# Kernel tuning notes

Hardware: AMD Instinct MI355X
Metric: run time of the kernel (lower is better)

Reference implementation:

```python
import jax, jax.numpy as jnp
import numpy as np

B, C_IN, C_OUT, E, H, W = 64, 384, 384, 8, 28, 28


def setup_inputs() -> dict:
    key = jax.random.key(0)
    k1, k2, k3 = jax.random.split(key, 3)
    x = jax.random.normal(k1, (B, C_IN, H, W), dtype=jnp.float32)
    routing_weights = jax.random.uniform(k2, (B, E), dtype=jnp.float32)
    # kaiming_normal_(mode='fan_out') per expert: std = sqrt(2 / fan_out), fan_out = out_channels * 1 * 1
    std = float(np.sqrt(2.0 / C_OUT))
    weight = jax.random.normal(k3, (E, C_OUT, C_IN), dtype=jnp.float32) * std
    return {"x": x, "routing_weights": routing_weights, "weight": weight}


def reference(x, routing_weights, weight):
    # Per-sample aggregated 1x1 conv weights: [b, c_out, c_in]
    agg = jnp.einsum('be,eoi->boi', routing_weights, weight)
    # Per-sample channel mixing (1x1 conv with groups=b == batched GEMM)
    out = jnp.einsum('boi,bihw->bohw', agg, x)
    return out
```

## Files before the change

### kernel.cpp

```cpp
#include <hip/hip_runtime.h>
#include <cstdint>

#define B_   64
#define CI_  384
#define CO_  384
#define HW_  784
#define E_   8
#define G_   (CI_ / 8)

typedef unsigned short ushort_t;
typedef unsigned int   uint_t;

typedef __attribute__((ext_vector_type(8))) short bf16x8;
typedef __attribute__((ext_vector_type(4))) float f32x4;

__device__ __forceinline__ ushort_t f2bf_rne(float f) {
  uint_t u = __builtin_bit_cast(uint_t, f);
  u += 0x7fffu + ((u >> 16) & 1u);
  return (ushort_t)(u >> 16);
}

__device__ __forceinline__ uint_t pack_bf16_trunc(float f0, float f1) {
  return __builtin_amdgcn_perm(__builtin_bit_cast(uint_t, f1),
                               __builtin_bit_cast(uint_t, f0),
                               0x07060302u);
}

#define AGG_BLOCKS 288
#define XQ_BLOCKS  (G_ * B_)

__global__ __launch_bounds__(256) void prep(const float* __restrict__ rw,
                                            const float* __restrict__ w,
                                            const float* __restrict__ x,
                                            ushort_t* __restrict__ agg,
                                            ushort_t* __restrict__ xq) {
  __shared__ float r[B_ * E_];
  const int blk = blockIdx.x;
  const int tid = threadIdx.x;

  if (blk < AGG_BLOCKS) {
    r[tid]       = rw[tid];
    r[tid + 256] = rw[tid + 256];
    const int base = blk * 512 + tid * 2;
    float2 wv[E_];
#pragma unroll
    for (int e = 0; e < E_; ++e)
      wv[e] = *(const float2*)&w[e * (CO_ * CI_) + base];
    __syncthreads();
#pragma unroll 8
    for (int b = 0; b < B_; ++b) {
      float ax = 0.f, ay = 0.f;
#pragma unroll
      for (int e = 0; e < E_; ++e) {
        const float rv = r[b * E_ + e];
        ax += rv * wv[e].x;
        ay += rv * wv[e].y;
      }
      const uint_t v = (uint_t)f2bf_rne(ax) | ((uint_t)f2bf_rne(ay) << 16);
      *(uint_t*)&agg[(size_t)b * (CO_ * CI_) + base] = v;
    }
  } else {
    const int idx = blk - AGG_BLOCKS;
    const int g = idx % G_;
    const int b = idx / G_;
    const float* xp = x + ((size_t)b * CI_ + g * 8) * HW_;
    ushort_t* op = xq + (((size_t)b * G_ + g) * HW_) * 8;
#pragma unroll
    for (int c = 0; c < 4; ++c) {
      const int hw = c * 256 + tid;
      if (hw < HW_) {
        float v[8];
#pragma unroll
        for (int j = 0; j < 8; ++j) v[j] = xp[(size_t)j * HW_ + hw];
        uint4 u;
        u.x = pack_bf16_trunc(v[0], v[1]);
        u.y = pack_bf16_trunc(v[2], v[3]);
        u.z = pack_bf16_trunc(v[4], v[5]);
        u.w = pack_bf16_trunc(v[6], v[7]);
        *(uint4*)&op[hw * 8] = u;
      }
    }
  }
}

#define BM 128
#define BN 128
#define BK 32
#define KIT (CI_ / BK)

__global__ __launch_bounds__(256, 4) void moe_gemm3(const ushort_t* __restrict__ Agg,
                                                    const ushort_t* __restrict__ Xq,
                                                    float* __restrict__ Out) {
  __shared__ __align__(16) ushort_t As[2][BM * BK];
  __shared__ __align__(16) ushort_t Bs[2][BN * BK];

  const int tid  = threadIdx.x;
  const int lane = tid & 63;
  const int wave = tid >> 6;
  const int wm = wave & 1, wn = wave >> 1;

  const int bx = blockIdx.x;
  const int by = blockIdx.y;
  const int bg  = by / 21;
  const int rem = by - bg * 21;
  const int mt  = rem / 7;
  const int nt  = rem - mt * 7;
  const int b   = bg * 8 + bx;

  const int sr0 = tid >> 2,          sq0 = (tid & 3) ^ ((tid >> 3) & 3);
  const int sr1 = (tid + 256) >> 2,  sq1 = (tid & 3) ^ (((tid + 256) >> 3) & 3);

  const ushort_t* Ab = Agg + (size_t)b * CO_ * CI_ + (size_t)(mt * BM) * CI_;
  const ushort_t* Asrc0 = Ab + sr0 * CI_ + sq0 * 8;
  const ushort_t* Asrc1 = Ab + sr1 * CI_ + sq1 * 8;

  int hw0 = nt * BN + sr0; hw0 = hw0 < HW_ ? hw0 : HW_ - 1;
  int hw1 = nt * BN + sr1; hw1 = hw1 < HW_ ? hw1 : HW_ - 1;
  const ushort_t* Xb = Xq + (size_t)b * G_ * HW_ * 8;
  const ushort_t* Bsrc0 = Xb + ((size_t)sq0 * HW_ + hw0) * 8;
  const ushort_t* Bsrc1 = Xb + ((size_t)sq1 * HW_ + hw1) * 8;

  const int l15 = lane & 15;
  const int lq  = lane >> 4;
  const int xqA = lq ^ ((l15 >> 1) & 3);

  f32x4 acc[4][4];
#pragma unroll
  for (int i = 0; i < 4; ++i)
#pragma unroll
    for (int j = 0; j < 4; ++j)
      acc[i][j] = (f32x4)0.f;

#define STAGE(PB, KK)                                                          \
  {                                                                            \
    __builtin_amdgcn_global_load_lds(                                          \
        (const __attribute__((address_space(1))) uint_t*)(Asrc0 + (KK) * BK),  \
        (__attribute__((address_space(3))) uint_t*)&As[PB][tid * 8], 16, 0, 0);\
    __builtin_amdgcn_global_load_lds(                                          \
        (const __attribute__((address_space(1))) uint_t*)(Asrc1 + (KK) * BK),  \
        (__attribute__((address_space(3))) uint_t*)&As[PB][(tid + 256) * 8],   \
        16, 0, 0);                                                             \
    const size_t bo_ = (size_t)(KK) * (4 * HW_ * 8);                           \
    __builtin_amdgcn_global_load_lds(                                          \
        (const __attribute__((address_space(1))) uint_t*)(Bsrc0 + bo_),        \
        (__attribute__((address_space(3))) uint_t*)&Bs[PB][tid * 8], 16, 0, 0);\
    __builtin_amdgcn_global_load_lds(                                          \
        (const __attribute__((address_space(1))) uint_t*)(Bsrc1 + bo_),        \
        (__attribute__((address_space(3))) uint_t*)&Bs[PB][(tid + 256) * 8],   \
        16, 0, 0);                                                             \
  }

  STAGE(0, 0);
  __syncthreads();

#pragma unroll 1
  for (int kk = 0; kk < KIT; ++kk) {
    const int buf = kk & 1;
    if (kk + 1 < KIT) STAGE(1 - buf, kk + 1);

    bf16x8 a[4], bb[4];
#pragma unroll
    for (int mf = 0; mf < 4; ++mf) {
      const int row = wm * 64 + mf * 16 + l15;
      a[mf] = *(const bf16x8*)&As[buf][(row * 4 + xqA) * 8];
    }
#pragma unroll
    for (int nf = 0; nf < 4; ++nf) {
      const int col = wn * 64 + nf * 16 + l15;
      bb[nf] = *(const bf16x8*)&Bs[buf][(col * 4 + xqA) * 8];
    }
#pragma unroll
    for (int mf = 0; mf < 4; ++mf)
#pragma unroll
      for (int nf = 0; nf < 4; ++nf)
        acc[mf][nf] = __builtin_amdgcn_mfma_f32_16x16x32_bf16(a[mf], bb[nf],
                                                              acc[mf][nf], 0, 0, 0);
    __syncthreads();
  }

  float* Ob = Out + (size_t)b * CO_ * HW_;
#pragma unroll
  for (int mf = 0; mf < 4; ++mf) {
#pragma unroll
    for (int nf = 0; nf < 4; ++nf) {
      const int n = nt * BN + wn * 64 + nf * 16 + l15;
      if (n < HW_) {
        const int mbase = mt * BM + wm * 64 + mf * 16 + lq * 4;
#pragma unroll
        for (int r = 0; r < 4; ++r)
          Ob[(size_t)(mbase + r) * HW_ + n] = acc[mf][nf][r];
      }
    }
  }
}

extern "C" void kernel_launch(void* const* d_in, const int* in_sizes, int n_in,
                              void* d_out, int out_size, void* d_ws, size_t ws_size,
                              hipStream_t stream) {
  const float* x  = (const float*)d_in[0];
  const float* rw = (const float*)d_in[1];
  const float* w  = (const float*)d_in[2];
  float* out = (float*)d_out;

  ushort_t* agg = (ushort_t*)d_ws;
  ushort_t* xq  = agg + (size_t)B_ * CO_ * CI_;

  prep<<<AGG_BLOCKS + XQ_BLOCKS, 256, 0, stream>>>(rw, w, x, agg, xq);
  moe_gemm3<<<dim3(8, 21 * (B_ / 8)), 256, 0, stream>>>(agg, xq, out);
}
```

Measured before the change: 173.6 us.

## Triple-buffer GEMM K-loop with explicit vmcnt waits and MFMA priority

Replaces the double-buffered K loop with a three-stage LDS ring that keeps two tile loads in flight. Each iteration waits on vmcnt and uses a single barrier in place of two __syncthreads, and the fully unrolled loop uses sched_barrier fences. s_setprio is raised around the MFMA block so matrix work is favoured while loads are pending. The cost is 1.5x the LDS per block and a lower occupancy hint (3 blocks per CU instead of 4).

```diff
diff --git a/kernel.cpp b/kernel.cpp
--- a/kernel.cpp
+++ b/kernel.cpp
@@ -88,11 +88,11 @@
 #define BK 32
 #define KIT (CI_ / BK)
 
-__global__ __launch_bounds__(256, 4) void moe_gemm3(const ushort_t* __restrict__ Agg,
+__global__ __launch_bounds__(256, 3) void moe_gemm4(const ushort_t* __restrict__ Agg,
                                                     const ushort_t* __restrict__ Xq,
                                                     float* __restrict__ Out) {
-  __shared__ __align__(16) ushort_t As[2][BM * BK];
-  __shared__ __align__(16) ushort_t Bs[2][BN * BK];
+  __shared__ __align__(16) ushort_t As[3][BM * BK];
+  __shared__ __align__(16) ushort_t Bs[3][BN * BK];
 
   const int tid  = threadIdx.x;
   const int lane = tid & 63;
@@ -150,33 +150,53 @@
         16, 0, 0);                                                             \
   }
 
+#define COMPUTE(CB)                                                            \
+  {                                                                            \
+    bf16x8 a[4], bb[4];                                                        \
+    _Pragma("unroll") for (int mf = 0; mf < 4; ++mf) {                         \
+      const int row = wm * 64 + mf * 16 + l15;                                 \
+      a[mf] = *(const bf16x8*)&As[CB][(row * 4 + xqA) * 8];                    \
+    }                                                                          \
+    _Pragma("unroll") for (int nf = 0; nf < 4; ++nf) {                         \
+      const int col = wn * 64 + nf * 16 + l15;                                 \
+      bb[nf] = *(const bf16x8*)&Bs[CB][(col * 4 + xqA) * 8];                   \
+    }                                                                          \
+    __builtin_amdgcn_s_setprio(1);                                             \
+    _Pragma("unroll") for (int mf = 0; mf < 4; ++mf)                           \
+      _Pragma("unroll") for (int nf = 0; nf < 4; ++nf)                         \
+        acc[mf][nf] = __builtin_amdgcn_mfma_f32_16x16x32_bf16(a[mf], bb[nf],   \
+                                                              acc[mf][nf],     \
+                                                              0, 0, 0);        \
+    __builtin_amdgcn_s_setprio(0);                                             \
+  }
+
+#define ITER_S(VM, CB, STG)                                                    \
+  {                                                                            \
+    asm volatile("s_waitcnt vmcnt(" #VM ")" ::: "memory");                     \
+    __builtin_amdgcn_s_barrier();                                              \
+    __builtin_amdgcn_sched_barrier(0);                                         \
+    STAGE((STG) % 3, STG);                                                     \
+    COMPUTE(CB);                                                               \
+    __builtin_amdgcn_sched_barrier(0);                                         \
+  }
+#define ITER_N(VM, CB)                                                         \
+  {                                                                            \
+    asm volatile("s_waitcnt vmcnt(" #VM ")" ::: "memory");                     \
+    __builtin_amdgcn_s_barrier();                                              \
+    __builtin_amdgcn_sched_barrier(0);                                         \
+    COMPUTE(CB);                                                               \
+    __builtin_amdgcn_sched_barrier(0);                                         \
+  }
+
   STAGE(0, 0);
-  __syncthreads();
-
-#pragma unroll 1
-  for (int kk = 0; kk < KIT; ++kk) {
-    const int buf = kk & 1;
-    if (kk + 1 < KIT) STAGE(1 - buf, kk + 1);
-
-    bf16x8 a[4], bb[4];
-#pragma unroll
-    for (int mf = 0; mf < 4; ++mf) {
-      const int row = wm * 64 + mf * 16 + l15;
-      a[mf] = *(const bf16x8*)&As[buf][(row * 4 + xqA) * 8];
-    }
-#pragma unroll
-    for (int nf = 0; nf < 4; ++nf) {
-      const int col = wn * 64 + nf * 16 + l15;
-      bb[nf] = *(const bf16x8*)&Bs[buf][(col * 4 + xqA) * 8];
-    }
-#pragma unroll
-    for (int mf = 0; mf < 4; ++mf)
-#pragma unroll
-      for (int nf = 0; nf < 4; ++nf)
-        acc[mf][nf] = __builtin_amdgcn_mfma_f32_16x16x32_bf16(a[mf], bb[nf],
-                                                              acc[mf][nf], 0, 0, 0);
-    __syncthreads();
-  }
+  STAGE(1, 1);
+
+#pragma unroll
+  for (int t = 0; t < 10; ++t)
+    ITER_S(4, t % 3, t + 2);
+
+  ITER_N(4, 1);
+  ITER_N(0, 2);
 
   float* Ob = Out + (size_t)b * CO_ * HW_;
 #pragma unroll
@@ -206,5 +226,5 @@
   ushort_t* xq  = agg + (size_t)B_ * CO_ * CI_;
 
   prep<<<AGG_BLOCKS + XQ_BLOCKS, 256, 0, stream>>>(rw, w, x, agg, xq);
-  moe_gemm3<<<dim3(8, 21 * (B_ / 8)), 256, 0, stream>>>(agg, xq, out);
-}
+  moe_gemm4<<<dim3(8, 21 * (B_ / 8)), 256, 0, stream>>>(agg, xq, out);
+}
```

New measurement: 170.5 us. No clear change (-1.8%).
